# Performance work log

Hardware: AMD Instinct MI355X
Metric: run time of the kernel (lower is better)

Reference implementation:

```python
import jax, jax.numpy as jnp
import numpy as np


def setup_inputs() -> dict:
    key = jax.random.key(0)
    k1, k2, k3, k4 = jax.random.split(key, 4)
    B, H, N, D = 4, 16, 2048, 128
    return {
        "q": jax.random.normal(k1, (B, H, N, D), dtype=jnp.float32),
        "k": jax.random.normal(k2, (B, H, N, D), dtype=jnp.float32),
        "v": jax.random.normal(k3, (B, H, N, D), dtype=jnp.float32),
        "g": jax.random.normal(k4, (B, H, N, 1), dtype=jnp.float32),
    }


def reference(q, k, v, g):
    """GLA recurrence: S_t = l_t * S_{t-1} + (1 - l_t) * k_t v_t^T; o_t = q_t S_t."""
    scale = 1.0
    B, H, N, D = q.shape
    lambd = jax.nn.sigmoid(g)                      # [B,H,N,1]
    qs = q * scale
    # time-major for scan: [N,B,H,...]
    qt = jnp.moveaxis(qs, 2, 0)
    kt = jnp.moveaxis(k, 2, 0)
    vt = jnp.moveaxis(v, 2, 0)
    lt = jnp.moveaxis(lambd, 2, 0)[..., None]      # [N,B,H,1,1]
    S0 = jnp.zeros((B, H, D, D), dtype=q.dtype)

    def step(S, inp):
        q_t, k_t, v_t, l_t = inp
        kv = jnp.einsum('bhd,bhe->bhde', k_t, v_t)  # rank-1 update per head
        S = l_t * S + (1.0 - l_t) * kv
        o = jnp.einsum('bhd,bhde->bhe', q_t, S)
        return S, o

    _, outs = jax.lax.scan(step, S0, (qt, kt, vt, lt))  # outs: [N,B,H,D]
    return jnp.moveaxis(outs, 0, 2)                     # [B,H,N,D]
```

## Files before the change

kernel.cpp:

```cpp
#include <hip/hip_runtime.h>

#define NTOK 2048
#define DD   128
#define CHK  64
#define NCH  32
#define EW   32

typedef __attribute__((ext_vector_type(8))) short bf16x8;
typedef __attribute__((ext_vector_type(4))) float f32x4;
typedef unsigned short u16;
typedef unsigned int u32;

#define MFMA(a,b,c) __builtin_amdgcn_mfma_f32_16x16x32_bf16(a,b,c,0,0,0)

__device__ __forceinline__ u16 f2bf(float f){
  union { float f; unsigned u; } x; x.f = f;
  return (u16)((x.u + 0x7fffu + ((x.u >> 16) & 1u)) >> 16);
}
__device__ __forceinline__ int swz(int r, int c, int re){
  int b = (r*re + c)*2;
  return b ^ ((r & 7) << 4);
}
__device__ __forceinline__ void lds_w1(u16* a, int r, int c, int re, u16 v){
  *(u16*)((char*)a + swz(r,c,re)) = v;
}
__device__ __forceinline__ void lds_w4(u16* a, int r, int c, int re, ushort4 v){
  *(ushort4*)((char*)a + swz(r,c,re)) = v;
}
__device__ __forceinline__ bf16x8 lds_r8(const u16* a, int r, int c, int re){
  return *(const bf16x8*)((const char*)a + swz(r,c,re));
}
__device__ __forceinline__ void gld16(const float* g, float* l){
  __builtin_amdgcn_global_load_lds((const __attribute__((address_space(1))) u32*)g,
                                   (__attribute__((address_space(3))) u32*)l, 16, 0, 0);
}
__device__ __forceinline__ void gld4(const float* g, float* l){
  __builtin_amdgcn_global_load_lds((const __attribute__((address_space(1))) u32*)g,
                                   (__attribute__((address_space(3))) u32*)l, 4, 0, 0);
}

__global__ __launch_bounds__(256) void gla_fused(
    const float* __restrict__ Qg, const float* __restrict__ Kg,
    const float* __restrict__ Vg, const float* __restrict__ Gg,
    float* __restrict__ Og)
{
  __shared__ float Kraw[CHK*DD];
  __shared__ float Vraw[CHK*EW];
  __shared__ float Graw[CHK];
  __shared__ u16 Kh [CHK*DD];
  __shared__ u16 KhT[DD*CHK];
  __shared__ u16 VT [EW*CHK];
  __shared__ u16 ST [EW*DD];
  __shared__ u16 Pb [CHK*CHK];

  const int tid = threadIdx.x;
  const int w = tid >> 6, l = tid & 63, lr = l & 15, lh = l >> 4;
  const int slot = blockIdx.x >> 3;
  const int bh = (blockIdx.x & 7) + 8*(slot >> 2);
  const int e0 = (slot & 3) * EW;

  const float* Qh  = Qg + (size_t)bh*NTOK*DD;
  const float* Kgh = Kg + (size_t)bh*NTOK*DD;
  const float* Vh  = Vg + (size_t)bh*NTOK*DD;
  const float* Gh  = Gg + (size_t)bh*NTOK;
  float* Oh = Og + (size_t)bh*NTOK*DD;

  f32x4 S00 = {}, S01 = {}, S10 = {}, S11 = {};
  float4 qpre[8];

  auto prefetch = [&](int c){
    const int t0 = c*CHK;
    #pragma unroll
    for (int i=0;i<8;++i){
      int u = i*256 + tid;
      int s = u >> 5, cu = u & 31;
      int src = (cu & 24) | ((cu & 7) ^ (s & 7));
      gld16(Kgh + (size_t)(t0+s)*DD + src*4, Kraw + u*4);
    }
    #pragma unroll
    for (int i=0;i<2;++i){
      int u = i*256 + tid;
      int s = u >> 3, sub = u & 7;
      gld16(Vh + (size_t)(t0+s)*DD + e0 + ((sub ^ (s&7))*4), Vraw + u*4);
    }
    if (w == 0) gld4(Gh + t0 + l, Graw + l);
    const float* qp = Qh + (size_t)(t0 + w*16 + lr)*DD + lh*8;
    #pragma unroll
    for (int ks=0;ks<4;++ks){
      qpre[ks*2]   = *(const float4*)(qp + ks*32);
      qpre[ks*2+1] = *(const float4*)(qp + ks*32 + 4);
    }
  };

  prefetch(0);

  for (int c=0; c<NCH; ++c){
    __syncthreads();

    float gv = Graw[l];
    float li = 1.f/(1.f + expf(-gv));
    float x  = log2f(li);
    #pragma unroll
    for (int off=1; off<64; off<<=1){
      float y = __shfl_up(x, off, 64);
      if (l >= off) x += y;
    }
    const float bl  = x;
    const float ckl = exp2f(-bl) * (1.f - li);
    const float cq  = exp2f(__shfl(bl, w*16 + lr, 64));
    const float scc = exp2f(__shfl(bl, 63, 64));

    #pragma unroll
    for (int i=0;i<8;++i){
      float4 kf = *(const float4*)(Kraw + l*DD + w*32 + ((i ^ (l&7)) * 4));
      int d = w*32 + i*4;
      u16 b0=f2bf(kf.x*ckl), b1=f2bf(kf.y*ckl), b2=f2bf(kf.z*ckl), b3=f2bf(kf.w*ckl);
      lds_w4(Kh, l, d, DD, make_ushort4(b0,b1,b2,b3));
      lds_w1(KhT, d+0, l, CHK, b0);
      lds_w1(KhT, d+1, l, CHK, b1);
      lds_w1(KhT, d+2, l, CHK, b2);
      lds_w1(KhT, d+3, l, CHK, b3);
    }
    #pragma unroll
    for (int j=0;j<2;++j){
      float4 vf = *(const float4*)(Vraw + l*EW + (((w*2+j) ^ (l&7)) * 4));
      int e = w*8 + j*4;
      lds_w1(VT, e+0, l, CHK, f2bf(vf.x));
      lds_w1(VT, e+1, l, CHK, f2bf(vf.y));
      lds_w1(VT, e+2, l, CHK, f2bf(vf.z));
      lds_w1(VT, e+3, l, CHK, f2bf(vf.w));
    }
    {
      const int dbase = w*32 + lh*4;
      #pragma unroll
      for (int r=0;r<4;++r){
        lds_w1(ST, lr,    dbase + r,      DD, f2bf(S00[r]));
        lds_w1(ST, 16+lr, dbase + r,      DD, f2bf(S01[r]));
        lds_w1(ST, lr,    dbase + 16 + r, DD, f2bf(S10[r]));
        lds_w1(ST, 16+lr, dbase + 16 + r, DD, f2bf(S11[r]));
      }
    }
    bf16x8 qA[4];
    #pragma unroll
    for (int ks=0;ks<4;++ks){
      float4 a = qpre[ks*2], b = qpre[ks*2+1];
      bf16x8 t;
      t[0]=(short)f2bf(a.x*cq); t[1]=(short)f2bf(a.y*cq);
      t[2]=(short)f2bf(a.z*cq); t[3]=(short)f2bf(a.w*cq);
      t[4]=(short)f2bf(b.x*cq); t[5]=(short)f2bf(b.y*cq);
      t[6]=(short)f2bf(b.z*cq); t[7]=(short)f2bf(b.w*cq);
      qA[ks] = t;
    }
    __syncthreads();
    if (c+1 < NCH) prefetch(c+1);

    f32x4 oacc0 = {}, oacc1 = {};
    f32x4 p0 = {}, p1 = {}, p2 = {}, p3 = {};
    #pragma unroll
    for (int ks=0;ks<4;++ks){
      const int kk = ks*32 + lh*8;
      bf16x8 a = qA[ks];
      oacc0 = MFMA(a, lds_r8(ST, lr,    kk, DD), oacc0);
      oacc1 = MFMA(a, lds_r8(ST, 16+lr, kk, DD), oacc1);
      p0 = MFMA(a, lds_r8(Kh, lr,    kk, DD), p0);
      p1 = MFMA(a, lds_r8(Kh, 16+lr, kk, DD), p1);
      p2 = MFMA(a, lds_r8(Kh, 32+lr, kk, DD), p2);
      p3 = MFMA(a, lds_r8(Kh, 48+lr, kk, DD), p3);
    }
    {
      const int t = w*16 + lh*4;
      #pragma unroll
      for (int r=0;r<4;++r){
        int tt = t + r;
        lds_w1(Pb, tt, lr,    CHK, f2bf((lr    <= tt) ? p0[r] : 0.f));
        lds_w1(Pb, tt, 16+lr, CHK, f2bf((16+lr <= tt) ? p1[r] : 0.f));
        lds_w1(Pb, tt, 32+lr, CHK, f2bf((32+lr <= tt) ? p2[r] : 0.f));
        lds_w1(Pb, tt, 48+lr, CHK, f2bf((48+lr <= tt) ? p3[r] : 0.f));
      }
    }
    __syncthreads();

    #pragma unroll
    for (int k2=0;k2<2;++k2){
      const int kk = k2*32 + lh*8;
      bf16x8 vb0 = lds_r8(VT, lr,    kk, CHK);
      bf16x8 vb1 = lds_r8(VT, 16+lr, kk, CHK);
      bf16x8 pa  = lds_r8(Pb, w*16 + lr, kk, CHK);
      oacc0 = MFMA(pa, vb0, oacc0);
      oacc1 = MFMA(pa, vb1, oacc1);
      bf16x8 ka0 = lds_r8(KhT, w*32 + lr,      kk, CHK);
      bf16x8 ka1 = lds_r8(KhT, w*32 + 16 + lr, kk, CHK);
      S00 = MFMA(ka0, vb0, S00);
      S01 = MFMA(ka0, vb1, S01);
      S10 = MFMA(ka1, vb0, S10);
      S11 = MFMA(ka1, vb1, S11);
    }
    #pragma unroll
    for (int r=0;r<4;++r){ S00[r]*=scc; S01[r]*=scc; S10[r]*=scc; S11[r]*=scc; }

    {
      float* op = Oh + (size_t)(c*CHK + w*16 + lh*4)*DD + e0;
      #pragma unroll
      for (int r=0;r<4;++r){
        op[r*DD + lr]      = oacc0[r];
        op[r*DD + 16 + lr] = oacc1[r];
      }
    }
  }
}

extern "C" void kernel_launch(void* const* d_in, const int* in_sizes, int n_in,
                              void* d_out, int out_size, void* d_ws, size_t ws_size,
                              hipStream_t stream)
{
  const float* q = (const float*)d_in[0];
  const float* k = (const float*)d_in[1];
  const float* v = (const float*)d_in[2];
  const float* g = (const float*)d_in[3];
  float* out = (float*)d_out;

  gla_fused<<<dim3(256), dim3(256), 0, stream>>>(q, k, v, g, out);
}
```

Before: 122.0 us.

## Split value dimension into 16-wide slices and double the grid

Halves the per-block value slice width, so the kernel launches twice as many blocks and allows two blocks per CU. Each block keeps less state in registers and does fewer MFMAs per chunk, while the QK^T and K conversion work is repeated across more blocks. V and gate values are now loaded into registers instead of through LDS. The barrier before the P·V and state update is replaced by a wave-local LDS wait, since each wave reads back only the Pb rows it wrote itself.

New measurement: 137.3 us. 12.5% more time.

```diff
diff --git a/kernel.cpp b/kernel.cpp
--- a/kernel.cpp
+++ b/kernel.cpp
@@ -4,7 +4,7 @@
 #define DD   128
 #define CHK  64
 #define NCH  32
-#define EW   32
+#define EW   16
 
 typedef __attribute__((ext_vector_type(8))) short bf16x8;
 typedef __attribute__((ext_vector_type(4))) float f32x4;
@@ -34,19 +34,13 @@
   __builtin_amdgcn_global_load_lds((const __attribute__((address_space(1))) u32*)g,
                                    (__attribute__((address_space(3))) u32*)l, 16, 0, 0);
 }
-__device__ __forceinline__ void gld4(const float* g, float* l){
-  __builtin_amdgcn_global_load_lds((const __attribute__((address_space(1))) u32*)g,
-                                   (__attribute__((address_space(3))) u32*)l, 4, 0, 0);
-}
-
-__global__ __launch_bounds__(256) void gla_fused(
+
+__global__ __launch_bounds__(256, 2) void gla_fused(
     const float* __restrict__ Qg, const float* __restrict__ Kg,
     const float* __restrict__ Vg, const float* __restrict__ Gg,
     float* __restrict__ Og)
 {
   __shared__ float Kraw[CHK*DD];
-  __shared__ float Vraw[CHK*EW];
-  __shared__ float Graw[CHK];
   __shared__ u16 Kh [CHK*DD];
   __shared__ u16 KhT[DD*CHK];
   __shared__ u16 VT [EW*CHK];
@@ -55,9 +49,8 @@
 
   const int tid = threadIdx.x;
   const int w = tid >> 6, l = tid & 63, lr = l & 15, lh = l >> 4;
-  const int slot = blockIdx.x >> 3;
-  const int bh = (blockIdx.x & 7) + 8*(slot >> 2);
-  const int e0 = (slot & 3) * EW;
+  const int bh = (blockIdx.x & 7) | (((blockIdx.x >> 6) & 7) << 3);
+  const int e0 = ((blockIdx.x >> 3) & 7) * EW;
 
   const float* Qh  = Qg + (size_t)bh*NTOK*DD;
   const float* Kgh = Kg + (size_t)bh*NTOK*DD;
@@ -65,8 +58,10 @@
   const float* Gh  = Gg + (size_t)bh*NTOK;
   float* Oh = Og + (size_t)bh*NTOK*DD;
 
-  f32x4 S00 = {}, S01 = {}, S10 = {}, S11 = {};
+  f32x4 S00 = {}, S10 = {};
   float4 qpre[8];
+  float4 vst;
+  float  gst;
 
   auto prefetch = [&](int c){
     const int t0 = c*CHK;
@@ -77,13 +72,8 @@
       int src = (cu & 24) | ((cu & 7) ^ (s & 7));
       gld16(Kgh + (size_t)(t0+s)*DD + src*4, Kraw + u*4);
     }
-    #pragma unroll
-    for (int i=0;i<2;++i){
-      int u = i*256 + tid;
-      int s = u >> 3, sub = u & 7;
-      gld16(Vh + (size_t)(t0+s)*DD + e0 + ((sub ^ (s&7))*4), Vraw + u*4);
-    }
-    if (w == 0) gld4(Gh + t0 + l, Graw + l);
+    vst = *(const float4*)(Vh + (size_t)(t0 + (tid>>2))*DD + e0 + (tid&3)*4);
+    gst = Gh[t0 + l];
     const float* qp = Qh + (size_t)(t0 + w*16 + lr)*DD + lh*8;
     #pragma unroll
     for (int ks=0;ks<4;++ks){
@@ -97,8 +87,7 @@
   for (int c=0; c<NCH; ++c){
     __syncthreads();
 
-    float gv = Graw[l];
-    float li = 1.f/(1.f + expf(-gv));
+    float li = 1.f/(1.f + expf(-gst));
     float x  = log2f(li);
     #pragma unroll
     for (int off=1; off<64; off<<=1){
@@ -121,23 +110,19 @@
       lds_w1(KhT, d+2, l, CHK, b2);
       lds_w1(KhT, d+3, l, CHK, b3);
     }
-    #pragma unroll
-    for (int j=0;j<2;++j){
-      float4 vf = *(const float4*)(Vraw + l*EW + (((w*2+j) ^ (l&7)) * 4));
-      int e = w*8 + j*4;
-      lds_w1(VT, e+0, l, CHK, f2bf(vf.x));
-      lds_w1(VT, e+1, l, CHK, f2bf(vf.y));
-      lds_w1(VT, e+2, l, CHK, f2bf(vf.z));
-      lds_w1(VT, e+3, l, CHK, f2bf(vf.w));
+    {
+      const int s = tid >> 2, eb = (tid & 3)*4;
+      lds_w1(VT, eb+0, s, CHK, f2bf(vst.x));
+      lds_w1(VT, eb+1, s, CHK, f2bf(vst.y));
+      lds_w1(VT, eb+2, s, CHK, f2bf(vst.z));
+      lds_w1(VT, eb+3, s, CHK, f2bf(vst.w));
     }
     {
       const int dbase = w*32 + lh*4;
       #pragma unroll
       for (int r=0;r<4;++r){
-        lds_w1(ST, lr,    dbase + r,      DD, f2bf(S00[r]));
-        lds_w1(ST, 16+lr, dbase + r,      DD, f2bf(S01[r]));
-        lds_w1(ST, lr,    dbase + 16 + r, DD, f2bf(S10[r]));
-        lds_w1(ST, 16+lr, dbase + 16 + r, DD, f2bf(S11[r]));
+        lds_w1(ST, lr, dbase + r,      DD, f2bf(S00[r]));
+        lds_w1(ST, lr, dbase + 16 + r, DD, f2bf(S10[r]));
       }
     }
     bf16x8 qA[4];
@@ -154,14 +139,13 @@
     __syncthreads();
     if (c+1 < NCH) prefetch(c+1);
 
-    f32x4 oacc0 = {}, oacc1 = {};
+    f32x4 oacc = {};
     f32x4 p0 = {}, p1 = {}, p2 = {}, p3 = {};
     #pragma unroll
     for (int ks=0;ks<4;++ks){
       const int kk = ks*32 + lh*8;
       bf16x8 a = qA[ks];
-      oacc0 = MFMA(a, lds_r8(ST, lr,    kk, DD), oacc0);
-      oacc1 = MFMA(a, lds_r8(ST, 16+lr, kk, DD), oacc1);
+      oacc = MFMA(a, lds_r8(ST, lr, kk, DD), oacc);
       p0 = MFMA(a, lds_r8(Kh, lr,    kk, DD), p0);
       p1 = MFMA(a, lds_r8(Kh, 16+lr, kk, DD), p1);
       p2 = MFMA(a, lds_r8(Kh, 32+lr, kk, DD), p2);
@@ -178,33 +162,27 @@
         lds_w1(Pb, tt, 48+lr, CHK, f2bf((48+lr <= tt) ? p3[r] : 0.f));
       }
     }
-    __syncthreads();
+    asm volatile("s_waitcnt lgkmcnt(0)" ::: "memory");
+    __builtin_amdgcn_sched_barrier(0);
 
     #pragma unroll
     for (int k2=0;k2<2;++k2){
       const int kk = k2*32 + lh*8;
-      bf16x8 vb0 = lds_r8(VT, lr,    kk, CHK);
-      bf16x8 vb1 = lds_r8(VT, 16+lr, kk, CHK);
+      bf16x8 vb  = lds_r8(VT, lr, kk, CHK);
       bf16x8 pa  = lds_r8(Pb, w*16 + lr, kk, CHK);
-      oacc0 = MFMA(pa, vb0, oacc0);
-      oacc1 = MFMA(pa, vb1, oacc1);
+      oacc = MFMA(pa, vb, oacc);
       bf16x8 ka0 = lds_r8(KhT, w*32 + lr,      kk, CHK);
       bf16x8 ka1 = lds_r8(KhT, w*32 + 16 + lr, kk, CHK);
-      S00 = MFMA(ka0, vb0, S00);
-      S01 = MFMA(ka0, vb1, S01);
-      S10 = MFMA(ka1, vb0, S10);
-      S11 = MFMA(ka1, vb1, S11);
-    }
-    #pragma unroll
-    for (int r=0;r<4;++r){ S00[r]*=scc; S01[r]*=scc; S10[r]*=scc; S11[r]*=scc; }
+      S00 = MFMA(ka0, vb, S00);
+      S10 = MFMA(ka1, vb, S10);
+    }
+    #pragma unroll
+    for (int r=0;r<4;++r){ S00[r]*=scc; S10[r]*=scc; }
 
     {
       float* op = Oh + (size_t)(c*CHK + w*16 + lh*4)*DD + e0;
       #pragma unroll
-      for (int r=0;r<4;++r){
-        op[r*DD + lr]      = oacc0[r];
-        op[r*DD + 16 + lr] = oacc1[r];
-      }
+      for (int r=0;r<4;++r) op[r*DD + lr] = oacc[r];
     }
   }
 }
@@ -219,5 +197,5 @@
   const float* g = (const float*)d_in[3];
   float* out = (float*)d_out;
 
-  gla_fused<<<dim3(256), dim3(256), 0, stream>>>(q, k, v, g, out);
-}
+  gla_fused<<<dim3(512), dim3(256), 0, stream>>>(q, k, v, g, out);
+}
```

## Split GLA sequence into two halves with midpoint state fixup kernel

Applied to the files above, without the earlier changes.

Splits each head's 2048-token recurrence into two independent halves run by separate blocks, which doubles the grid and halves the serial chunk chain. The first half stores its final state, and the second half records cumulative log-decay prefixes. A second kernel then adds q·S_mid, scaled by the decay, into the outputs of the second half. The change also swaps the global_load_lds staging for register prefetch and replaces the mid-loop block barrier with an LDS waitcnt. The cost is a second launch, an extra read of Q for the second half and a read-modify-write of the output.

After: 140.8 us. +15.4%, slower.

```diff
diff --git a/kernel.cpp b/kernel.cpp
--- a/kernel.cpp
+++ b/kernel.cpp
@@ -3,13 +3,12 @@
 #define NTOK 2048
 #define DD   128
 #define CHK  64
-#define NCH  32
+#define PCH  16
 #define EW   32
 
 typedef __attribute__((ext_vector_type(8))) short bf16x8;
 typedef __attribute__((ext_vector_type(4))) float f32x4;
 typedef unsigned short u16;
-typedef unsigned int u32;
 
 #define MFMA(a,b,c) __builtin_amdgcn_mfma_f32_16x16x32_bf16(a,b,c,0,0,0)
 
@@ -30,120 +29,113 @@
 __device__ __forceinline__ bf16x8 lds_r8(const u16* a, int r, int c, int re){
   return *(const bf16x8*)((const char*)a + swz(r,c,re));
 }
-__device__ __forceinline__ void gld16(const float* g, float* l){
-  __builtin_amdgcn_global_load_lds((const __attribute__((address_space(1))) u32*)g,
-                                   (__attribute__((address_space(3))) u32*)l, 16, 0, 0);
-}
-__device__ __forceinline__ void gld4(const float* g, float* l){
-  __builtin_amdgcn_global_load_lds((const __attribute__((address_space(1))) u32*)g,
-                                   (__attribute__((address_space(3))) u32*)l, 4, 0, 0);
-}
-
-__global__ __launch_bounds__(256) void gla_fused(
+
+__global__ __launch_bounds__(256) void gla_part(
     const float* __restrict__ Qg, const float* __restrict__ Kg,
     const float* __restrict__ Vg, const float* __restrict__ Gg,
-    float* __restrict__ Og)
+    float* __restrict__ Og, float* __restrict__ Smid, float* __restrict__ Bpre)
 {
-  __shared__ float Kraw[CHK*DD];
-  __shared__ float Vraw[CHK*EW];
-  __shared__ float Graw[CHK];
-  __shared__ u16 Kh [CHK*DD];
-  __shared__ u16 KhT[DD*CHK];
-  __shared__ u16 VT [EW*CHK];
-  __shared__ u16 ST [EW*DD];
-  __shared__ u16 Pb [CHK*CHK];
+  __shared__ u16 sKh [CHK*DD];
+  __shared__ u16 sKhT[DD*CHK];
+  __shared__ u16 sVT [EW*CHK];
+  __shared__ u16 sST [EW*DD];
+  __shared__ u16 sPb [CHK*CHK];
 
   const int tid = threadIdx.x;
   const int w = tid >> 6, l = tid & 63, lr = l & 15, lh = l >> 4;
-  const int slot = blockIdx.x >> 3;
-  const int bh = (blockIdx.x & 7) + 8*(slot >> 2);
-  const int e0 = (slot & 3) * EW;
-
-  const float* Qh  = Qg + (size_t)bh*NTOK*DD;
-  const float* Kgh = Kg + (size_t)bh*NTOK*DD;
-  const float* Vh  = Vg + (size_t)bh*NTOK*DD;
-  const float* Gh  = Gg + (size_t)bh*NTOK;
-  float* Oh = Og + (size_t)bh*NTOK*DD;
+  const int gid  = blockIdx.x;
+  const int head = (gid & 7) | (((gid >> 6) & 7) << 3);
+  const int e0   = ((gid >> 3) & 3) * EW;
+  const int part = (gid >> 5) & 1;
+  const int tbase = part * (PCH*CHK);
+
+  const float* Qh = Qg + (size_t)head*NTOK*DD;
+  const float* Kh = Kg + (size_t)head*NTOK*DD;
+  const float* Vh = Vg + (size_t)head*NTOK*DD;
+  const float* Gh = Gg + (size_t)head*NTOK;
+  float* Oh = Og + (size_t)head*NTOK*DD;
 
   f32x4 S00 = {}, S01 = {}, S10 = {}, S11 = {};
-  float4 qpre[8];
-
-  auto prefetch = [&](int c){
-    const int t0 = c*CHK;
-    #pragma unroll
-    for (int i=0;i<8;++i){
-      int u = i*256 + tid;
-      int s = u >> 5, cu = u & 31;
-      int src = (cu & 24) | ((cu & 7) ^ (s & 7));
-      gld16(Kgh + (size_t)(t0+s)*DD + src*4, Kraw + u*4);
-    }
-    #pragma unroll
-    for (int i=0;i<2;++i){
-      int u = i*256 + tid;
-      int s = u >> 3, sub = u & 7;
-      gld16(Vh + (size_t)(t0+s)*DD + e0 + ((sub ^ (s&7))*4), Vraw + u*4);
-    }
-    if (w == 0) gld4(Gh + t0 + l, Graw + l);
+  float4 kpre[8], vpre[2], qpre[8];
+  float gst;
+
+  auto loads = [&](int c){
+    const int t0 = tbase + c*CHK;
+    gst = Gh[t0 + l];
+    const int srow = t0 + (tid >> 2);
+    const float* kp = Kh + (size_t)srow*DD + 4*(tid & 3);
+    #pragma unroll
+    for (int i=0;i<8;++i) kpre[i] = *(const float4*)(kp + 16*i);
+    const float* vp = Vh + (size_t)srow*DD + e0 + 4*(tid & 3);
+    #pragma unroll
+    for (int i=0;i<2;++i) vpre[i] = *(const float4*)(vp + 16*i);
     const float* qp = Qh + (size_t)(t0 + w*16 + lr)*DD + lh*8;
     #pragma unroll
-    for (int ks=0;ks<4;++ks){
-      qpre[ks*2]   = *(const float4*)(qp + ks*32);
-      qpre[ks*2+1] = *(const float4*)(qp + ks*32 + 4);
+    for (int i=0;i<4;++i){
+      qpre[2*i]   = *(const float4*)(qp + 32*i);
+      qpre[2*i+1] = *(const float4*)(qp + 32*i + 4);
     }
   };
 
-  prefetch(0);
-
-  for (int c=0; c<NCH; ++c){
-    __syncthreads();
-
-    float gv = Graw[l];
-    float li = 1.f/(1.f + expf(-gv));
+  float ckl_s, cq, scc, bl63;
+  auto scan = [&](){
+    float li = 1.f/(1.f + expf(-gst));
     float x  = log2f(li);
     #pragma unroll
     for (int off=1; off<64; off<<=1){
       float y = __shfl_up(x, off, 64);
       if (l >= off) x += y;
     }
-    const float bl  = x;
-    const float ckl = exp2f(-bl) * (1.f - li);
-    const float cq  = exp2f(__shfl(bl, w*16 + lr, 64));
-    const float scc = exp2f(__shfl(bl, 63, 64));
-
+    bl63 = __shfl(x, 63, 64);
+    scc  = exp2f(bl63);
+    cq   = exp2f(__shfl(x, w*16 + lr, 64));
+    float cklr = exp2f(-x) * (1.f - li);
+    ckl_s = __shfl(cklr, w*16 + (l >> 2), 64);
+  };
+
+  loads(0);
+  scan();
+  float bsum = 0.f;
+  if (part == 1 && e0 == 0 && tid == 0) Bpre[head*PCH] = 0.f;
+
+  for (int c=0; c<PCH; ++c){
+    __syncthreads();
+
+    const int srow = tid >> 2;
     #pragma unroll
     for (int i=0;i<8;++i){
-      float4 kf = *(const float4*)(Kraw + l*DD + w*32 + ((i ^ (l&7)) * 4));
-      int d = w*32 + i*4;
-      u16 b0=f2bf(kf.x*ckl), b1=f2bf(kf.y*ckl), b2=f2bf(kf.z*ckl), b3=f2bf(kf.w*ckl);
-      lds_w4(Kh, l, d, DD, make_ushort4(b0,b1,b2,b3));
-      lds_w1(KhT, d+0, l, CHK, b0);
-      lds_w1(KhT, d+1, l, CHK, b1);
-      lds_w1(KhT, d+2, l, CHK, b2);
-      lds_w1(KhT, d+3, l, CHK, b3);
-    }
-    #pragma unroll
-    for (int j=0;j<2;++j){
-      float4 vf = *(const float4*)(Vraw + l*EW + (((w*2+j) ^ (l&7)) * 4));
-      int e = w*8 + j*4;
-      lds_w1(VT, e+0, l, CHK, f2bf(vf.x));
-      lds_w1(VT, e+1, l, CHK, f2bf(vf.y));
-      lds_w1(VT, e+2, l, CHK, f2bf(vf.z));
-      lds_w1(VT, e+3, l, CHK, f2bf(vf.w));
+      float4 kf = kpre[i];
+      int d = 4*((tid & 3) + 4*i);
+      u16 b0=f2bf(kf.x*ckl_s), b1=f2bf(kf.y*ckl_s), b2=f2bf(kf.z*ckl_s), b3=f2bf(kf.w*ckl_s);
+      lds_w4(sKh, srow, d, DD, make_ushort4(b0,b1,b2,b3));
+      lds_w1(sKhT, d+0, srow, CHK, b0);
+      lds_w1(sKhT, d+1, srow, CHK, b1);
+      lds_w1(sKhT, d+2, srow, CHK, b2);
+      lds_w1(sKhT, d+3, srow, CHK, b3);
+    }
+    #pragma unroll
+    for (int i=0;i<2;++i){
+      float4 vf = vpre[i];
+      int e = 4*((tid & 3) + 4*i);
+      lds_w1(sVT, e+0, srow, CHK, f2bf(vf.x));
+      lds_w1(sVT, e+1, srow, CHK, f2bf(vf.y));
+      lds_w1(sVT, e+2, srow, CHK, f2bf(vf.z));
+      lds_w1(sVT, e+3, srow, CHK, f2bf(vf.w));
     }
     {
       const int dbase = w*32 + lh*4;
       #pragma unroll
       for (int r=0;r<4;++r){
-        lds_w1(ST, lr,    dbase + r,      DD, f2bf(S00[r]));
-        lds_w1(ST, 16+lr, dbase + r,      DD, f2bf(S01[r]));
-        lds_w1(ST, lr,    dbase + 16 + r, DD, f2bf(S10[r]));
-        lds_w1(ST, 16+lr, dbase + 16 + r, DD, f2bf(S11[r]));
+        lds_w1(sST, lr,    dbase + r,      DD, f2bf(S00[r]));
+        lds_w1(sST, 16+lr, dbase + r,      DD, f2bf(S01[r]));
+        lds_w1(sST, lr,    dbase + 16 + r, DD, f2bf(S10[r]));
+        lds_w1(sST, 16+lr, dbase + 16 + r, DD, f2bf(S11[r]));
       }
     }
     bf16x8 qA[4];
     #pragma unroll
     for (int ks=0;ks<4;++ks){
-      float4 a = qpre[ks*2], b = qpre[ks*2+1];
+      float4 a = qpre[2*ks], b = qpre[2*ks+1];
       bf16x8 t;
       t[0]=(short)f2bf(a.x*cq); t[1]=(short)f2bf(a.y*cq);
       t[2]=(short)f2bf(a.z*cq); t[3]=(short)f2bf(a.w*cq);
@@ -151,8 +143,8 @@
       t[6]=(short)f2bf(b.z*cq); t[7]=(short)f2bf(b.w*cq);
       qA[ks] = t;
     }
+    if (c+1 < PCH) loads(c+1);
     __syncthreads();
-    if (c+1 < NCH) prefetch(c+1);
 
     f32x4 oacc0 = {}, oacc1 = {};
     f32x4 p0 = {}, p1 = {}, p2 = {}, p3 = {};
@@ -160,36 +152,37 @@
     for (int ks=0;ks<4;++ks){
       const int kk = ks*32 + lh*8;
       bf16x8 a = qA[ks];
-      oacc0 = MFMA(a, lds_r8(ST, lr,    kk, DD), oacc0);
-      oacc1 = MFMA(a, lds_r8(ST, 16+lr, kk, DD), oacc1);
-      p0 = MFMA(a, lds_r8(Kh, lr,    kk, DD), p0);
-      p1 = MFMA(a, lds_r8(Kh, 16+lr, kk, DD), p1);
-      p2 = MFMA(a, lds_r8(Kh, 32+lr, kk, DD), p2);
-      p3 = MFMA(a, lds_r8(Kh, 48+lr, kk, DD), p3);
+      oacc0 = MFMA(a, lds_r8(sST, lr,    kk, DD), oacc0);
+      oacc1 = MFMA(a, lds_r8(sST, 16+lr, kk, DD), oacc1);
+      p0 = MFMA(a, lds_r8(sKh, lr,    kk, DD), p0);
+      p1 = MFMA(a, lds_r8(sKh, 16+lr, kk, DD), p1);
+      p2 = MFMA(a, lds_r8(sKh, 32+lr, kk, DD), p2);
+      p3 = MFMA(a, lds_r8(sKh, 48+lr, kk, DD), p3);
     }
     {
       const int t = w*16 + lh*4;
       #pragma unroll
       for (int r=0;r<4;++r){
         int tt = t + r;
-        lds_w1(Pb, tt, lr,    CHK, f2bf((lr    <= tt) ? p0[r] : 0.f));
-        lds_w1(Pb, tt, 16+lr, CHK, f2bf((16+lr <= tt) ? p1[r] : 0.f));
-        lds_w1(Pb, tt, 32+lr, CHK, f2bf((32+lr <= tt) ? p2[r] : 0.f));
-        lds_w1(Pb, tt, 48+lr, CHK, f2bf((48+lr <= tt) ? p3[r] : 0.f));
+        lds_w1(sPb, tt, lr,    CHK, f2bf((lr    <= tt) ? p0[r] : 0.f));
+        lds_w1(sPb, tt, 16+lr, CHK, f2bf((16+lr <= tt) ? p1[r] : 0.f));
+        lds_w1(sPb, tt, 32+lr, CHK, f2bf((32+lr <= tt) ? p2[r] : 0.f));
+        lds_w1(sPb, tt, 48+lr, CHK, f2bf((48+lr <= tt) ? p3[r] : 0.f));
       }
     }
-    __syncthreads();
+    asm volatile("s_waitcnt lgkmcnt(0)" ::: "memory");
+    __builtin_amdgcn_sched_barrier(0);
 
     #pragma unroll
     for (int k2=0;k2<2;++k2){
       const int kk = k2*32 + lh*8;
-      bf16x8 vb0 = lds_r8(VT, lr,    kk, CHK);
-      bf16x8 vb1 = lds_r8(VT, 16+lr, kk, CHK);
-      bf16x8 pa  = lds_r8(Pb, w*16 + lr, kk, CHK);
+      bf16x8 vb0 = lds_r8(sVT, lr,    kk, CHK);
+      bf16x8 vb1 = lds_r8(sVT, 16+lr, kk, CHK);
+      bf16x8 pa  = lds_r8(sPb, w*16 + lr, kk, CHK);
       oacc0 = MFMA(pa, vb0, oacc0);
       oacc1 = MFMA(pa, vb1, oacc1);
-      bf16x8 ka0 = lds_r8(KhT, w*32 + lr,      kk, CHK);
-      bf16x8 ka1 = lds_r8(KhT, w*32 + 16 + lr, kk, CHK);
+      bf16x8 ka0 = lds_r8(sKhT, w*32 + lr,      kk, CHK);
+      bf16x8 ka1 = lds_r8(sKhT, w*32 + 16 + lr, kk, CHK);
       S00 = MFMA(ka0, vb0, S00);
       S01 = MFMA(ka0, vb1, S01);
       S10 = MFMA(ka1, vb0, S10);
@@ -199,13 +192,108 @@
     for (int r=0;r<4;++r){ S00[r]*=scc; S01[r]*=scc; S10[r]*=scc; S11[r]*=scc; }
 
     {
-      float* op = Oh + (size_t)(c*CHK + w*16 + lh*4)*DD + e0;
+      float* op = Oh + (size_t)(tbase + c*CHK + w*16 + lh*4)*DD + e0;
       #pragma unroll
       for (int r=0;r<4;++r){
         op[r*DD + lr]      = oacc0[r];
         op[r*DD + 16 + lr] = oacc1[r];
       }
     }
+    if (c+1 < PCH){
+      if (part == 1){
+        bsum += bl63;
+        if (e0 == 0 && tid == 0) Bpre[head*PCH + c + 1] = bsum;
+      }
+      scan();
+    }
+  }
+
+  if (part == 0){
+    float* sm = Smid + (size_t)head*DD*DD + e0;
+    const int dbase = w*32 + lh*4;
+    #pragma unroll
+    for (int r=0;r<4;++r){
+      sm[(size_t)(dbase + r)*DD + lr]           = S00[r];
+      sm[(size_t)(dbase + r)*DD + 16 + lr]      = S01[r];
+      sm[(size_t)(dbase + 16 + r)*DD + lr]      = S10[r];
+      sm[(size_t)(dbase + 16 + r)*DD + 16 + lr] = S11[r];
+    }
+  }
+}
+
+__global__ __launch_bounds__(256) void gla_fix(
+    const float* __restrict__ Qg, const float* __restrict__ Gg,
+    float* __restrict__ Og, const float* __restrict__ Smid,
+    const float* __restrict__ Bpre)
+{
+  __shared__ u16 sS[DD*DD];
+  const int tid = threadIdx.x;
+  const int w = tid >> 6, l = tid & 63, lr = l & 15, lh = l >> 4;
+  const int head = blockIdx.x >> 4, c = blockIdx.x & 15;
+  const int t0 = PCH*CHK + c*CHK;
+
+  {
+    const int d = tid >> 1, eb = (tid & 1)*64;
+    const float* sp = Smid + (size_t)head*DD*DD + (size_t)d*DD + eb;
+    #pragma unroll
+    for (int j=0;j<16;++j){
+      float4 f = *(const float4*)(sp + 4*j);
+      lds_w1(sS, eb + 4*j + 0, d, DD, f2bf(f.x));
+      lds_w1(sS, eb + 4*j + 1, d, DD, f2bf(f.y));
+      lds_w1(sS, eb + 4*j + 2, d, DD, f2bf(f.z));
+      lds_w1(sS, eb + 4*j + 3, d, DD, f2bf(f.w));
+    }
+  }
+  float gst = Gg[(size_t)head*NTOK + t0 + l];
+  float li = 1.f/(1.f + expf(-gst));
+  float x  = log2f(li);
+  #pragma unroll
+  for (int off=1; off<64; off<<=1){
+    float y = __shfl_up(x, off, 64);
+    if (l >= off) x += y;
+  }
+  const float cq = exp2f(__shfl(x, w*16 + lr, 64) + Bpre[head*PCH + c]);
+
+  bf16x8 qA[4];
+  const float* qp = Qg + (size_t)head*NTOK*DD + (size_t)(t0 + w*16 + lr)*DD + lh*8;
+  #pragma unroll
+  for (int ks=0;ks<4;++ks){
+    float4 a = *(const float4*)(qp + ks*32);
+    float4 b = *(const float4*)(qp + ks*32 + 4);
+    bf16x8 t;
+    t[0]=(short)f2bf(a.x*cq); t[1]=(short)f2bf(a.y*cq);
+    t[2]=(short)f2bf(a.z*cq); t[3]=(short)f2bf(a.w*cq);
+    t[4]=(short)f2bf(b.x*cq); t[5]=(short)f2bf(b.y*cq);
+    t[6]=(short)f2bf(b.z*cq); t[7]=(short)f2bf(b.w*cq);
+    qA[ks] = t;
+  }
+  __syncthreads();
+
+  f32x4 o0={},o1={},o2={},o3={},o4={},o5={},o6={},o7={};
+  #pragma unroll
+  for (int ks=0;ks<4;++ks){
+    const int kk = ks*32 + lh*8;
+    bf16x8 a = qA[ks];
+    o0 = MFMA(a, lds_r8(sS, lr,      kk, DD), o0);
+    o1 = MFMA(a, lds_r8(sS, 16+lr,   kk, DD), o1);
+    o2 = MFMA(a, lds_r8(sS, 32+lr,   kk, DD), o2);
+    o3 = MFMA(a, lds_r8(sS, 48+lr,   kk, DD), o3);
+    o4 = MFMA(a, lds_r8(sS, 64+lr,   kk, DD), o4);
+    o5 = MFMA(a, lds_r8(sS, 80+lr,   kk, DD), o5);
+    o6 = MFMA(a, lds_r8(sS, 96+lr,   kk, DD), o6);
+    o7 = MFMA(a, lds_r8(sS, 112+lr,  kk, DD), o7);
+  }
+  float* op = Og + (size_t)head*NTOK*DD + (size_t)(t0 + w*16 + lh*4)*DD;
+  #pragma unroll
+  for (int r=0;r<4;++r){
+    op[r*DD + lr]       += o0[r];
+    op[r*DD + 16 + lr]  += o1[r];
+    op[r*DD + 32 + lr]  += o2[r];
+    op[r*DD + 48 + lr]  += o3[r];
+    op[r*DD + 64 + lr]  += o4[r];
+    op[r*DD + 80 + lr]  += o5[r];
+    op[r*DD + 96 + lr]  += o6[r];
+    op[r*DD + 112 + lr] += o7[r];
   }
 }
 
@@ -218,6 +306,9 @@
   const float* v = (const float*)d_in[2];
   const float* g = (const float*)d_in[3];
   float* out = (float*)d_out;
-
-  gla_fused<<<dim3(256), dim3(256), 0, stream>>>(q, k, v, g, out);
-}
+  float* Smid = (float*)d_ws;
+  float* Bpre = (float*)((char*)d_ws + (size_t)64*DD*DD*4);
+
+  gla_part<<<dim3(512),  dim3(256), 0, stream>>>(q, k, v, g, out, Smid, Bpre);
+  gla_fix <<<dim3(1024), dim3(256), 0, stream>>>(q, g, out, Smid, Bpre);
+}
```
